# Optimization experiments

Hardware: AMD Instinct MI355X
Metric: run time of the kernel (lower is better)

The kernel has to match this reference:

```python
import jax, jax.numpy as jnp
import numpy as np

NEG_INF = float(np.finfo(np.float32).min)
EPS = 1e-6
NOISE_STD = 1.0
CHUNK = 8
TEMP = 1.0


def moving_sum(x, back, forward):
    # x: [B, T]; windowed sum over [t-back, t+forward] via prefix sums (O(T))
    B, T = x.shape
    cs = jnp.concatenate([jnp.zeros((B, 1), x.dtype), jnp.cumsum(x, axis=1)], axis=1)  # [B, T+1]
    idx = jnp.arange(T)
    hi = jnp.clip(idx + forward + 1, 0, T)
    lo = jnp.clip(idx - back, 0, T)
    return cs[:, hi] - cs[:, lo]


def setup_inputs() -> dict:
    key = jax.random.key(0)
    ks = jax.random.split(key, 12)
    B, T, KD, QD, AD, VD = 16, 4000, 512, 512, 512, 512
    s = lambda d: 1.0 / np.sqrt(d)
    return {
        "key": jax.random.normal(ks[0], (B, T, KD), jnp.float32),
        "value": jax.random.normal(ks[1], (B, T, VD), jnp.float32),
        "query": jax.random.normal(ks[2], (B, 1, QD), jnp.float32),
        "mask": jnp.ones((B, 1, T), jnp.int32),
        "w_key_mono": jax.random.normal(ks[3], (KD, AD), jnp.float32) * s(KD),
        "b_key_mono": jnp.zeros((AD,), jnp.float32),
        "w_query_mono": jax.random.normal(ks[4], (QD, AD), jnp.float32) * s(QD),
        "v_mono": jax.random.normal(ks[5], (AD,), jnp.float32) * s(AD),
        "g_mono": jnp.asarray(np.sqrt(1.0 / AD), jnp.float32),  # weight_norm gain init
        "r_mono": jnp.asarray(-4.0, jnp.float32),
        "w_key_chunk": jax.random.normal(ks[6], (KD, AD), jnp.float32) * s(KD),
        "b_key_chunk": jnp.zeros((AD,), jnp.float32),
        "w_query_chunk": jax.random.normal(ks[7], (QD, AD), jnp.float32) * s(QD),
        "v_chunk": jax.random.normal(ks[8], (AD,), jnp.float32) * s(AD),
    }


def _energy(key, query, mask, wk, bk, wq, v, r=None, g=None):
    kproj = jax.nn.relu(key) @ wk + bk          # [B, T, A]
    qproj = query @ wq                           # [B, 1, A]
    if g is not None:  # weight-normalized v
        v = g * v / jnp.linalg.norm(v)
    e = jnp.tanh(kproj + qproj) @ v              # [B, T]
    if r is not None:
        e = e + r
    return jnp.where(mask[:, 0, :] == 0, NEG_INF, e)


def reference(key, value, query, mask, w_key_mono, b_key_mono, w_query_mono, v_mono,
              g_mono, r_mono, w_key_chunk, b_key_chunk, w_query_chunk, v_chunk):
    B, T, _ = key.shape
    e_mono = _energy(key, query, mask, w_key_mono, b_key_mono, w_query_mono,
                     v_mono, r=r_mono, g=g_mono)
    noise = jax.random.normal(jax.random.key(123), e_mono.shape, e_mono.dtype) * NOISE_STD
    p_choose = jax.nn.sigmoid(e_mono + noise)                      # [B, T]
    # safe_cumprod of (1 - p): exp(exclusive cumsum of clipped logs)
    log1mp = jnp.log(jnp.clip(1.0 - p_choose, EPS, 1.0))
    cumprod_1mp = jnp.exp(jnp.cumsum(log1mp, axis=1) - log1mp)     # exclusive
    aw_prev = jnp.zeros((B, T), key.dtype).at[:, 0].set(1.0)       # one-hot at t=0
    alpha = p_choose * cumprod_1mp * jnp.cumsum(
        aw_prev / jnp.clip(cumprod_1mp, EPS, 1.0), axis=1)
    # chunkwise attention
    e_chunk = _energy(key, query, mask, w_key_chunk, b_key_chunk, w_query_chunk, v_chunk)
    e_chunk = e_chunk - jnp.max(e_chunk, axis=1, keepdims=True)
    softmax_exp = jnp.maximum(jnp.exp(e_chunk), 1e-5)
    denom = moving_sum(softmax_exp, CHUNK - 1, 0)
    beta = softmax_exp * moving_sum(alpha * TEMP / denom, 0, CHUNK - 1)
    cv = jnp.einsum('bt,btd->bd', beta, value)[:, None, :]         # [B, 1, V]
    return cv, alpha[..., None]
```

## Files before the change

### kernel.cpp

```cpp
#include <hip/hip_runtime.h>
#include <stdint.h>

typedef unsigned short u16;
typedef unsigned int   u32;

#define T_LEN 4000
#define NEG_INF (-3.4028234663852886e38f)

typedef __bf16 bf16x8 __attribute__((ext_vector_type(8)));
typedef float  f32x4  __attribute__((ext_vector_type(4)));

__device__ __forceinline__ u16 f2bf(float f){
    union { float f; u32 i; } v; v.f = f;
    u32 u = v.i;
    u32 r = (u + 0x7FFFu + ((u >> 16) & 1u)) >> 16;
    return (u16)r;
}
__device__ __forceinline__ float tanh_fast(float x){
    float ax = fabsf(x);
    float a = __expf(-2.0f * ax);
    float t = (1.0f - a) / (1.0f + a);
    return copysignf(t, x);
}
__device__ __forceinline__ u32 rotl32(u32 x, int n){ return (x << n) | (x >> (32 - n)); }

__device__ float jax_noise(u32 idx){
    const u32 k0 = 0u, k1 = 123u;
    const u32 k2 = k0 ^ k1 ^ 0x1BD11BDAu;
    u32 x0 = k0;
    u32 x1 = idx + k1;
#define RND(r) { x0 += x1; x1 = rotl32(x1, r); x1 ^= x0; }
    RND(13) RND(15) RND(26) RND(6)   x0 += k1; x1 += k2 + 1u;
    RND(17) RND(29) RND(16) RND(24)  x0 += k2; x1 += k0 + 2u;
    RND(13) RND(15) RND(26) RND(6)   x0 += k0; x1 += k1 + 3u;
    RND(17) RND(29) RND(16) RND(24)  x0 += k1; x1 += k2 + 4u;
    RND(13) RND(15) RND(26) RND(6)   x0 += k2; x1 += k0 + 5u;
#undef RND
    u32 bits = x0 ^ x1;
    union { u32 i; float f; } u;
    u.i = (bits >> 9) | 0x3F800000u;
    float f01 = u.f - 1.0f;
    const float minval = -0.99999994f;
    float uu = f01 * (1.0f - minval) + minval;
    uu = fmaxf(uu, minval);
    return 1.41421356f * erfinvf(uu);
}

__global__ __launch_bounds__(512) void prep_all(
    const float* __restrict__ v_mono, const float* __restrict__ g_mono,
    const float* __restrict__ query, const float* __restrict__ wq_mono,
    const float* __restrict__ wq_chunk,
    const float* __restrict__ wk_mono, const float* __restrict__ wk_chunk,
    float* __restrict__ vn, float* __restrict__ qp_mono, float* __restrict__ qp_chunk,
    u16* __restrict__ Wt)
{
    __shared__ float shf[512];
    __shared__ u16 tile[32][33];
    const int blk = blockIdx.x;
    const int tid = threadIdx.x;
    if (blk == 0){
        float v = v_mono[tid];
        shf[tid] = v * v;
        __syncthreads();
        for (int off = 256; off >= 1; off >>= 1){
            if (tid < off) shf[tid] += shf[tid + off];
            __syncthreads();
        }
        float g = g_mono[0];
        vn[tid] = g * v / sqrtf(shf[0]);
    } else if (blk <= 32){
        int b = (blk - 1) >> 1;
        int which = (blk - 1) & 1;
        const float* W = which ? wq_chunk : wq_mono;
        float* out = which ? qp_chunk : qp_mono;
        shf[tid] = query[b * 512 + tid];
        __syncthreads();
        float acc = 0.f;
        for (int k = 0; k < 512; k++) acc += shf[k] * W[k * 512 + tid];
        out[b * 512 + tid] = acc;
    } else {
        int idx = blk - 33;
        int kt = (idx & 15) * 32, nt = (idx >> 4) * 32;
        int c = tid & 31, r = tid >> 5;
        const float* src = (nt < 512) ? wk_mono : wk_chunk;
        int nbase = (nt < 512) ? nt : nt - 512;
#pragma unroll
        for (int i = 0; i < 2; i++){
            int kk = r + i * 16;
            tile[kk][c] = f2bf(src[(size_t)(kt + kk) * 512 + nbase + c]);
        }
        __syncthreads();
#pragma unroll
        for (int i = 0; i < 2; i++){
            int nn = r + i * 16;
            Wt[(size_t)(nt + nn) * 512 + kt + c] = tile[c][nn];
        }
    }
}

__global__ __launch_bounds__(256) void prep_key(const float* __restrict__ key,
                                                u16* __restrict__ kb){
    size_t i = ((size_t)blockIdx.x * 256 + threadIdx.x) * 8;
    float4 a = *reinterpret_cast<const float4*>(key + i);
    float4 b = *reinterpret_cast<const float4*>(key + i + 4);
    uint4 pk;
    pk.x = (u32)f2bf(fmaxf(a.x, 0.f)) | ((u32)f2bf(fmaxf(a.y, 0.f)) << 16);
    pk.y = (u32)f2bf(fmaxf(a.z, 0.f)) | ((u32)f2bf(fmaxf(a.w, 0.f)) << 16);
    pk.z = (u32)f2bf(fmaxf(b.x, 0.f)) | ((u32)f2bf(fmaxf(b.y, 0.f)) << 16);
    pk.w = (u32)f2bf(fmaxf(b.z, 0.f)) | ((u32)f2bf(fmaxf(b.w, 0.f)) << 16);
    *reinterpret_cast<uint4*>(kb + i) = pk;
}

template<bool PRE>
__global__ __launch_bounds__(256) void gemm_energy(
    const float* __restrict__ key, const u16* __restrict__ kb,
    const u16* __restrict__ Wt,
    const float* __restrict__ b_mono, const float* __restrict__ b_chunk,
    const float* __restrict__ vnorm, const float* __restrict__ v_chunk,
    const float* __restrict__ qp_mono, const float* __restrict__ qp_chunk,
    float* __restrict__ e_mono, float* __restrict__ e_chunk)
{
    __shared__ __align__(16) u16 As[128 * 40];
    __shared__ __align__(16) u16 Bs[128 * 40];
    const int tid = threadIdx.x;
    const int g0 = blockIdx.x * 128;
    const int nT = blockIdx.y;
    const bool mono = (nT < 4);
    const int n0 = nT * 128;
    const int lane = tid & 63;
    const int wave = tid >> 6;
    const int wm = wave >> 1, wn = wave & 1;
    const int l15 = lane & 15, quad = lane >> 4;

    f32x4 acc[4][4];
#pragma unroll
    for (int i = 0; i < 4; i++)
#pragma unroll
        for (int j = 0; j < 4; j++)
#pragma unroll
            for (int c = 0; c < 4; c++) acc[i][j][c] = 0.f;

    for (int k0 = 0; k0 < 512; k0 += 32){
        __syncthreads();
        if (PRE){
#pragma unroll
            for (int it = 0; it < 2; it++){
                int vid = tid + it * 256;
                int row = vid >> 2;
                int cb  = (vid & 3) << 3;
                uint4 a = *reinterpret_cast<const uint4*>(kb + (size_t)(g0 + row) * 512 + k0 + cb);
                *reinterpret_cast<uint4*>(&As[row * 40 + cb]) = a;
            }
        } else {
#pragma unroll
            for (int it = 0; it < 4; it++){
                int vid = tid + it * 256;
                int row = vid >> 3;
                int c4  = (vid & 7) << 2;
                float4 a = *reinterpret_cast<const float4*>(key + (size_t)(g0 + row) * 512 + k0 + c4);
                u32 p0 = (u32)f2bf(fmaxf(a.x, 0.f)) | ((u32)f2bf(fmaxf(a.y, 0.f)) << 16);
                u32 p1 = (u32)f2bf(fmaxf(a.z, 0.f)) | ((u32)f2bf(fmaxf(a.w, 0.f)) << 16);
                uint2 pk; pk.x = p0; pk.y = p1;
                *reinterpret_cast<uint2*>(&As[row * 40 + c4]) = pk;
            }
        }
#pragma unroll
        for (int it = 0; it < 2; it++){
            int vid = tid + it * 256;
            int row = vid >> 2;
            int cb  = (vid & 3) << 3;
            uint4 b = *reinterpret_cast<const uint4*>(Wt + (size_t)(n0 + row) * 512 + k0 + cb);
            *reinterpret_cast<uint4*>(&Bs[row * 40 + cb]) = b;
        }
        __syncthreads();
        bf16x8 af[4], bfr[4];
#pragma unroll
        for (int i = 0; i < 4; i++){
            af[i]  = *reinterpret_cast<const bf16x8*>(&As[(wm * 64 + i * 16 + l15) * 40 + quad * 8]);
            bfr[i] = *reinterpret_cast<const bf16x8*>(&Bs[(wn * 64 + i * 16 + l15) * 40 + quad * 8]);
        }
#pragma unroll
        for (int i = 0; i < 4; i++)
#pragma unroll
            for (int j = 0; j < 4; j++)
                acc[i][j] = __builtin_amdgcn_mfma_f32_16x16x32_bf16(af[i], bfr[j], acc[i][j], 0, 0, 0);
    }

    const float* qp = mono ? qp_mono : qp_chunk;
    float* edst = mono ? e_mono : e_chunk;
    float vv[4], bb[4]; int nc[4];
#pragma unroll
    for (int j = 0; j < 4; j++){
        int ncol = (n0 - (mono ? 0 : 512)) + wn * 64 + j * 16 + l15;
        nc[j] = ncol;
        vv[j] = mono ? vnorm[ncol] : v_chunk[ncol];
        bb[j] = mono ? b_mono[ncol] : b_chunk[ncol];
    }
#pragma unroll
    for (int i = 0; i < 4; i++){
#pragma unroll
        for (int r = 0; r < 4; r++){
            int g = g0 + wm * 64 + i * 16 + quad * 4 + r;
            int bidx = (u32)g / 4000u;
            float s = 0.f;
#pragma unroll
            for (int j = 0; j < 4; j++){
                float x = acc[i][j][r] + bb[j] + qp[bidx * 512 + nc[j]];
                s += vv[j] * tanh_fast(x);
            }
            s += __shfl_xor(s, 1);
            s += __shfl_xor(s, 2);
            s += __shfl_xor(s, 4);
            s += __shfl_xor(s, 8);
            if (l15 == 0) atomicAdd(&edst[g], s);
        }
    }
}

__global__ __launch_bounds__(256) void scan_energy(
    const float* __restrict__ e_mono, const float* __restrict__ e_chunk,
    const int* __restrict__ mask, const float* __restrict__ r_mono,
    float* __restrict__ out_alpha, float* __restrict__ beta)
{
    __shared__ float P[T_LEN];
    __shared__ float AL[T_LEN];
    __shared__ float SE[T_LEN];
    __shared__ float red[256];
    const int b = blockIdx.x;
    const int tid = threadIdx.x;
    const float r = r_mono[0];
    const int t0 = tid * 16;

    float l[16];
    float lsum = 0.f;
#pragma unroll
    for (int i = 0; i < 16; i++){
        int t = t0 + i;
        if (t < T_LEN){
            int fl = b * T_LEN + t;
            float e = e_mono[fl] + r;
            if (mask[fl] == 0) e = NEG_INF;
            float x = e + jax_noise((u32)fl);
            float p = 1.0f / (1.0f + expf(-x));
            P[t] = p;
            float om = 1.0f - p;
            om = fminf(fmaxf(om, 1e-6f), 1.0f);
            l[i] = logf(om);
            lsum += l[i];
        } else l[i] = 0.f;
    }
    red[tid] = lsum;
    __syncthreads();
#pragma unroll
    for (int off = 1; off < 256; off <<= 1){
        float v = (tid >= off) ? red[tid - off] : 0.f;
        __syncthreads();
        red[tid] += v;
        __syncthreads();
    }
    float run = red[tid] - lsum;
#pragma unroll
    for (int i = 0; i < 16; i++){
        int t = t0 + i;
        if (t < T_LEN){
            float alpha = P[t] * expf(run);
            run += l[i];
            AL[t] = alpha;
            out_alpha[b * T_LEN + t] = alpha;
        }
    }

    float ec[16]; float lmax = NEG_INF;
#pragma unroll
    for (int i = 0; i < 16; i++){
        int t = t0 + i;
        if (t < T_LEN){
            int fl = b * T_LEN + t;
            float e = e_chunk[fl];
            if (mask[fl] == 0) e = NEG_INF;
            ec[i] = e;
            lmax = fmaxf(lmax, e);
        } else ec[i] = NEG_INF;
    }
    __syncthreads();
    red[tid] = lmax;
    __syncthreads();
    for (int off = 128; off >= 1; off >>= 1){
        if (tid < off) red[tid] = fmaxf(red[tid], red[tid + off]);
        __syncthreads();
    }
    float m = red[0];
#pragma unroll
    for (int i = 0; i < 16; i++){
        int t = t0 + i;
        if (t < T_LEN) SE[t] = fmaxf(expf(ec[i] - m), 1e-5f);
    }
    __syncthreads();
#pragma unroll
    for (int i = 0; i < 16; i++){
        int t = t0 + i;
        if (t < T_LEN){
            float d = 0.f;
            int lo = t - 7; if (lo < 0) lo = 0;
            for (int s = lo; s <= t; s++) d += SE[s];
            P[t] = AL[t] / d;
        }
    }
    __syncthreads();
#pragma unroll
    for (int i = 0; i < 16; i++){
        int t = t0 + i;
        if (t < T_LEN){
            float s2 = 0.f;
            int hi = t + 7; if (hi > T_LEN - 1) hi = T_LEN - 1;
            for (int s = t; s <= hi; s++) s2 += P[s];
            beta[b * T_LEN + t] = SE[t] * s2;
        }
    }
}

__global__ __launch_bounds__(256) void cv_accum(const float* __restrict__ value,
                                                const float* __restrict__ beta,
                                                float* __restrict__ outcv){
    const int b = blockIdx.x >> 4;
    const int c = blockIdx.x & 15;
    const int tid = threadIdx.x;
    __shared__ float bsh[250];
    int tstart = c * 250;
    if (tid < 250) bsh[tid] = beta[b * T_LEN + tstart + tid];
    __syncthreads();
    int dl = (tid & 127) * 4;
    int trow = tid >> 7;
    float4 a = {0.f, 0.f, 0.f, 0.f};
    for (int t = trow; t < 250; t += 2){
        float bt = bsh[t];
        float4 v = *reinterpret_cast<const float4*>(
            value + (size_t)(b * T_LEN + tstart + t) * 512 + dl);
        a.x += bt * v.x; a.y += bt * v.y; a.z += bt * v.z; a.w += bt * v.w;
    }
    atomicAdd(&outcv[b * 512 + dl + 0], a.x);
    atomicAdd(&outcv[b * 512 + dl + 1], a.y);
    atomicAdd(&outcv[b * 512 + dl + 2], a.z);
    atomicAdd(&outcv[b * 512 + dl + 3], a.w);
}

extern "C" void kernel_launch(void* const* d_in, const int* in_sizes, int n_in,
                              void* d_out, int out_size, void* d_ws, size_t ws_size,
                              hipStream_t stream)
{
    const float* key      = (const float*)d_in[0];
    const float* value    = (const float*)d_in[1];
    const float* query    = (const float*)d_in[2];
    const int*   mask     = (const int*)d_in[3];
    const float* wk_mono  = (const float*)d_in[4];
    const float* bk_mono  = (const float*)d_in[5];
    const float* wq_mono  = (const float*)d_in[6];
    const float* v_mono   = (const float*)d_in[7];
    const float* g_mono   = (const float*)d_in[8];
    const float* r_mono   = (const float*)d_in[9];
    const float* wk_chunk = (const float*)d_in[10];
    const float* bk_chunk = (const float*)d_in[11];
    const float* wq_chunk = (const float*)d_in[12];
    const float* v_chunk  = (const float*)d_in[13];

    float* ws      = (float*)d_ws;
    float* e_mono  = ws;
    float* e_chunk = ws + 64000;
    float* beta    = ws + 136192;
    float* qp_mono = ws + 200192;
    float* qp_chunk= ws + 208384;
    float* vnorm   = ws + 216576;
    u16*   Wt      = (u16*)(ws + 217088);
    u16*   kb      = (u16*)(ws + 479232);

    const size_t NEED = 479232u * 4u + (size_t)64000 * 512 * 2;
    const bool big = ws_size >= NEED;

    hipMemsetAsync(ws, 0, 128000 * sizeof(float), stream);
    hipMemsetAsync(d_out, 0, 8192 * sizeof(float), stream);

    prep_all<<<545, 512, 0, stream>>>(v_mono, g_mono, query, wq_mono, wq_chunk,
                                      wk_mono, wk_chunk, vnorm, qp_mono, qp_chunk, Wt);
    if (big){
        prep_key<<<16000, 256, 0, stream>>>(key, kb);
        gemm_energy<true><<<dim3(500, 8), 256, 0, stream>>>(key, kb, Wt, bk_mono, bk_chunk,
                                                            vnorm, v_chunk, qp_mono, qp_chunk,
                                                            e_mono, e_chunk);
    } else {
        gemm_energy<false><<<dim3(500, 8), 256, 0, stream>>>(key, kb, Wt, bk_mono, bk_chunk,
                                                             vnorm, v_chunk, qp_mono, qp_chunk,
                                                             e_mono, e_chunk);
    }
    scan_energy<<<16, 256, 0, stream>>>(e_mono, e_chunk, mask, r_mono,
                                        (float*)d_out + 8192, beta);
    cv_accum<<<256, 256, 0, stream>>>(value, beta, (float*)d_out);
}
```

Before: 516.4 us.

## Fuse prep kernels and memsets, use direct-to-LDS loads and swizzled GEMM grid

Merges the weight prep, key bf16 conversion and the two memsets into one launch, which removes several kernel and memset launches. The pre-converted GEMM path now loads A and B tiles with global_load_lds straight into unpadded LDS, and remaps block ids so groups of 8 row tiles share each of the 8 column tiles for better L2 reuse. The scan kernel pads its shared arrays to avoid bank conflicts. Risks: unpadded LDS tiles may cause bank conflicts on the fragment reads, and the single-buffered loop still waits on each load before computing.

```diff
diff --git a/kernel.cpp b/kernel.cpp
--- a/kernel.cpp
+++ b/kernel.cpp
@@ -23,6 +23,12 @@
     return copysignf(t, x);
 }
 __device__ __forceinline__ u32 rotl32(u32 x, int n){ return (x << n) | (x >> (32 - n)); }
+
+__device__ __forceinline__ void gll16(const void* g, void* l){
+    __builtin_amdgcn_global_load_lds(
+        (__attribute__((address_space(1))) void*)g,
+        (__attribute__((address_space(3))) void*)l, 16, 0, 0);
+}
 
 __device__ float jax_noise(u32 idx){
     const u32 k0 = 0u, k1 = 123u;
@@ -46,13 +52,15 @@
     return 1.41421356f * erfinvf(uu);
 }
 
-__global__ __launch_bounds__(512) void prep_all(
+__global__ __launch_bounds__(512) void prep_combined(
     const float* __restrict__ v_mono, const float* __restrict__ g_mono,
     const float* __restrict__ query, const float* __restrict__ wq_mono,
     const float* __restrict__ wq_chunk,
     const float* __restrict__ wk_mono, const float* __restrict__ wk_chunk,
+    const float* __restrict__ key,
     float* __restrict__ vn, float* __restrict__ qp_mono, float* __restrict__ qp_chunk,
-    u16* __restrict__ Wt)
+    u16* __restrict__ Wt, u16* __restrict__ kb,
+    float* __restrict__ ezero, float* __restrict__ outcv)
 {
     __shared__ float shf[512];
     __shared__ u16 tile[32][33];
@@ -78,7 +86,7 @@
         float acc = 0.f;
         for (int k = 0; k < 512; k++) acc += shf[k] * W[k * 512 + tid];
         out[b * 512 + tid] = acc;
-    } else {
+    } else if (blk <= 544){
         int idx = blk - 33;
         int kt = (idx & 15) * 32, nt = (idx >> 4) * 32;
         int c = tid & 31, r = tid >> 5;
@@ -95,26 +103,119 @@
             int nn = r + i * 16;
             Wt[(size_t)(nt + nn) * 512 + kt + c] = tile[c][nn];
         }
-    }
-}
-
-__global__ __launch_bounds__(256) void prep_key(const float* __restrict__ key,
-                                                u16* __restrict__ kb){
-    size_t i = ((size_t)blockIdx.x * 256 + threadIdx.x) * 8;
-    float4 a = *reinterpret_cast<const float4*>(key + i);
-    float4 b = *reinterpret_cast<const float4*>(key + i + 4);
-    uint4 pk;
-    pk.x = (u32)f2bf(fmaxf(a.x, 0.f)) | ((u32)f2bf(fmaxf(a.y, 0.f)) << 16);
-    pk.y = (u32)f2bf(fmaxf(a.z, 0.f)) | ((u32)f2bf(fmaxf(a.w, 0.f)) << 16);
-    pk.z = (u32)f2bf(fmaxf(b.x, 0.f)) | ((u32)f2bf(fmaxf(b.y, 0.f)) << 16);
-    pk.w = (u32)f2bf(fmaxf(b.z, 0.f)) | ((u32)f2bf(fmaxf(b.w, 0.f)) << 16);
-    *reinterpret_cast<uint4*>(kb + i) = pk;
-}
-
-template<bool PRE>
-__global__ __launch_bounds__(256) void gemm_energy(
-    const float* __restrict__ key, const u16* __restrict__ kb,
-    const u16* __restrict__ Wt,
+    } else if (blk < 608){
+        int i = ((blk - 545) * 512 + tid) * 4;
+        if (i < 128000){
+            float4 z = {0.f, 0.f, 0.f, 0.f};
+            *reinterpret_cast<float4*>(ezero + i) = z;
+        }
+    } else if (blk < 612){
+        int i = ((blk - 608) * 512 + tid) * 4;
+        float4 z = {0.f, 0.f, 0.f, 0.f};
+        *reinterpret_cast<float4*>(outcv + i) = z;
+    } else {
+        size_t i = ((size_t)(blk - 612) * 512 + tid) * 8;
+        float4 a = *reinterpret_cast<const float4*>(key + i);
+        float4 b = *reinterpret_cast<const float4*>(key + i + 4);
+        uint4 pk;
+        pk.x = (u32)f2bf(fmaxf(a.x, 0.f)) | ((u32)f2bf(fmaxf(a.y, 0.f)) << 16);
+        pk.y = (u32)f2bf(fmaxf(a.z, 0.f)) | ((u32)f2bf(fmaxf(a.w, 0.f)) << 16);
+        pk.z = (u32)f2bf(fmaxf(b.x, 0.f)) | ((u32)f2bf(fmaxf(b.y, 0.f)) << 16);
+        pk.w = (u32)f2bf(fmaxf(b.z, 0.f)) | ((u32)f2bf(fmaxf(b.w, 0.f)) << 16);
+        *reinterpret_cast<uint4*>(kb + i) = pk;
+    }
+}
+
+__global__ __launch_bounds__(256) void gemm_energy_pre(
+    const u16* __restrict__ kb, const u16* __restrict__ Wt,
+    const float* __restrict__ b_mono, const float* __restrict__ b_chunk,
+    const float* __restrict__ vnorm, const float* __restrict__ v_chunk,
+    const float* __restrict__ qp_mono, const float* __restrict__ qp_chunk,
+    float* __restrict__ e_mono, float* __restrict__ e_chunk)
+{
+    __shared__ __align__(16) u16 As[128 * 32];
+    __shared__ __align__(16) u16 Bs[128 * 32];
+    const int bid = blockIdx.x;
+    const int x = ((bid >> 6) << 3) + (bid & 7);
+    if (x >= 500) return;
+    const int nT = (bid >> 3) & 7;
+    const int g0 = x * 128;
+    const bool mono = (nT < 4);
+    const int n0 = nT * 128;
+    const int tid = threadIdx.x;
+    const int lane = tid & 63;
+    const int wave = tid >> 6;
+    const int wm = wave >> 1, wn = wave & 1;
+    const int l15 = lane & 15, quad = lane >> 4;
+
+    f32x4 acc[4][4];
+#pragma unroll
+    for (int i = 0; i < 4; i++)
+#pragma unroll
+        for (int j = 0; j < 4; j++)
+#pragma unroll
+            for (int c = 0; c < 4; c++) acc[i][j][c] = 0.f;
+
+    const u16* aG = kb + (size_t)g0 * 512;
+    const u16* bG = Wt + (size_t)n0 * 512;
+
+    for (int k0 = 0; k0 < 512; k0 += 32){
+#pragma unroll
+        for (int it = 0; it < 2; it++){
+            int vid = tid + it * 256;
+            int row = vid >> 2;
+            int part = vid & 3;
+            gll16(aG + (size_t)row * 512 + k0 + part * 8, As + vid * 8);
+            gll16(bG + (size_t)row * 512 + k0 + part * 8, Bs + vid * 8);
+        }
+        __syncthreads();
+        bf16x8 af[4], bfr[4];
+#pragma unroll
+        for (int i = 0; i < 4; i++){
+            af[i]  = *reinterpret_cast<const bf16x8*>(&As[(wm * 64 + i * 16 + l15) * 32 + quad * 8]);
+            bfr[i] = *reinterpret_cast<const bf16x8*>(&Bs[(wn * 64 + i * 16 + l15) * 32 + quad * 8]);
+        }
+#pragma unroll
+        for (int i = 0; i < 4; i++)
+#pragma unroll
+            for (int j = 0; j < 4; j++)
+                acc[i][j] = __builtin_amdgcn_mfma_f32_16x16x32_bf16(af[i], bfr[j], acc[i][j], 0, 0, 0);
+        __syncthreads();
+    }
+
+    const float* qp = mono ? qp_mono : qp_chunk;
+    float* edst = mono ? e_mono : e_chunk;
+    float vv[4], bb[4]; int nc[4];
+#pragma unroll
+    for (int j = 0; j < 4; j++){
+        int ncol = (n0 - (mono ? 0 : 512)) + wn * 64 + j * 16 + l15;
+        nc[j] = ncol;
+        vv[j] = mono ? vnorm[ncol] : v_chunk[ncol];
+        bb[j] = mono ? b_mono[ncol] : b_chunk[ncol];
+    }
+#pragma unroll
+    for (int i = 0; i < 4; i++){
+#pragma unroll
+        for (int r = 0; r < 4; r++){
+            int g = g0 + wm * 64 + i * 16 + quad * 4 + r;
+            int bidx = (u32)g / 4000u;
+            float s = 0.f;
+#pragma unroll
+            for (int j = 0; j < 4; j++){
+                float x2 = acc[i][j][r] + bb[j] + qp[bidx * 512 + nc[j]];
+                s += vv[j] * tanh_fast(x2);
+            }
+            s += __shfl_xor(s, 1);
+            s += __shfl_xor(s, 2);
+            s += __shfl_xor(s, 4);
+            s += __shfl_xor(s, 8);
+            if (l15 == 0) atomicAdd(&edst[g], s);
+        }
+    }
+}
+
+__global__ __launch_bounds__(256) void gemm_energy_f32(
+    const float* __restrict__ key, const u16* __restrict__ Wt,
     const float* __restrict__ b_mono, const float* __restrict__ b_chunk,
     const float* __restrict__ vnorm, const float* __restrict__ v_chunk,
     const float* __restrict__ qp_mono, const float* __restrict__ qp_chunk,
@@ -142,27 +243,16 @@
 
     for (int k0 = 0; k0 < 512; k0 += 32){
         __syncthreads();
-        if (PRE){
-#pragma unroll
-            for (int it = 0; it < 2; it++){
-                int vid = tid + it * 256;
-                int row = vid >> 2;
-                int cb  = (vid & 3) << 3;
-                uint4 a = *reinterpret_cast<const uint4*>(kb + (size_t)(g0 + row) * 512 + k0 + cb);
-                *reinterpret_cast<uint4*>(&As[row * 40 + cb]) = a;
-            }
-        } else {
-#pragma unroll
-            for (int it = 0; it < 4; it++){
-                int vid = tid + it * 256;
-                int row = vid >> 3;
-                int c4  = (vid & 7) << 2;
-                float4 a = *reinterpret_cast<const float4*>(key + (size_t)(g0 + row) * 512 + k0 + c4);
-                u32 p0 = (u32)f2bf(fmaxf(a.x, 0.f)) | ((u32)f2bf(fmaxf(a.y, 0.f)) << 16);
-                u32 p1 = (u32)f2bf(fmaxf(a.z, 0.f)) | ((u32)f2bf(fmaxf(a.w, 0.f)) << 16);
-                uint2 pk; pk.x = p0; pk.y = p1;
-                *reinterpret_cast<uint2*>(&As[row * 40 + c4]) = pk;
-            }
+#pragma unroll
+        for (int it = 0; it < 4; it++){
+            int vid = tid + it * 256;
+            int row = vid >> 3;
+            int c4  = (vid & 7) << 2;
+            float4 a = *reinterpret_cast<const float4*>(key + (size_t)(g0 + row) * 512 + k0 + c4);
+            u32 p0 = (u32)f2bf(fmaxf(a.x, 0.f)) | ((u32)f2bf(fmaxf(a.y, 0.f)) << 16);
+            u32 p1 = (u32)f2bf(fmaxf(a.z, 0.f)) | ((u32)f2bf(fmaxf(a.w, 0.f)) << 16);
+            uint2 pk; pk.x = p0; pk.y = p1;
+            *reinterpret_cast<uint2*>(&As[row * 40 + c4]) = pk;
         }
 #pragma unroll
         for (int it = 0; it < 2; it++){
@@ -217,14 +307,16 @@
     }
 }
 
+#define IDX(t) ((t) + ((t) >> 4))
+
 __global__ __launch_bounds__(256) void scan_energy(
     const float* __restrict__ e_mono, const float* __restrict__ e_chunk,
     const int* __restrict__ mask, const float* __restrict__ r_mono,
     float* __restrict__ out_alpha, float* __restrict__ beta)
 {
-    __shared__ float P[T_LEN];
-    __shared__ float AL[T_LEN];
-    __shared__ float SE[T_LEN];
+    __shared__ float P[4256];
+    __shared__ float AL[4256];
+    __shared__ float SE[4256];
     __shared__ float red[256];
     const int b = blockIdx.x;
     const int tid = threadIdx.x;
@@ -242,7 +334,7 @@
             if (mask[fl] == 0) e = NEG_INF;
             float x = e + jax_noise((u32)fl);
             float p = 1.0f / (1.0f + expf(-x));
-            P[t] = p;
+            P[IDX(t)] = p;
             float om = 1.0f - p;
             om = fminf(fmaxf(om, 1e-6f), 1.0f);
             l[i] = logf(om);
@@ -263,9 +355,9 @@
     for (int i = 0; i < 16; i++){
         int t = t0 + i;
         if (t < T_LEN){
-            float alpha = P[t] * expf(run);
+            float alpha = P[IDX(t)] * expf(run);
             run += l[i];
-            AL[t] = alpha;
+            AL[IDX(t)] = alpha;
             out_alpha[b * T_LEN + t] = alpha;
         }
     }
@@ -293,7 +385,7 @@
 #pragma unroll
     for (int i = 0; i < 16; i++){
         int t = t0 + i;
-        if (t < T_LEN) SE[t] = fmaxf(expf(ec[i] - m), 1e-5f);
+        if (t < T_LEN) SE[IDX(t)] = fmaxf(expf(ec[i] - m), 1e-5f);
     }
     __syncthreads();
 #pragma unroll
@@ -302,8 +394,8 @@
         if (t < T_LEN){
             float d = 0.f;
             int lo = t - 7; if (lo < 0) lo = 0;
-            for (int s = lo; s <= t; s++) d += SE[s];
-            P[t] = AL[t] / d;
+            for (int s = lo; s <= t; s++) d += SE[IDX(s)];
+            P[IDX(t)] = AL[IDX(t)] / d;
         }
     }
     __syncthreads();
@@ -313,8 +405,8 @@
         if (t < T_LEN){
             float s2 = 0.f;
             int hi = t + 7; if (hi > T_LEN - 1) hi = T_LEN - 1;
-            for (int s = t; s <= hi; s++) s2 += P[s];
-            beta[b * T_LEN + t] = SE[t] * s2;
+            for (int s = t; s <= hi; s++) s2 += P[IDX(s)];
+            beta[b * T_LEN + t] = SE[IDX(t)] * s2;
         }
     }
 }
@@ -376,20 +468,18 @@
     const size_t NEED = 479232u * 4u + (size_t)64000 * 512 * 2;
     const bool big = ws_size >= NEED;
 
-    hipMemsetAsync(ws, 0, 128000 * sizeof(float), stream);
-    hipMemsetAsync(d_out, 0, 8192 * sizeof(float), stream);
-
-    prep_all<<<545, 512, 0, stream>>>(v_mono, g_mono, query, wq_mono, wq_chunk,
-                                      wk_mono, wk_chunk, vnorm, qp_mono, qp_chunk, Wt);
+    prep_combined<<<big ? 8612 : 612, 512, 0, stream>>>(
+        v_mono, g_mono, query, wq_mono, wq_chunk, wk_mono, wk_chunk, key,
+        vnorm, qp_mono, qp_chunk, Wt, kb, e_mono, (float*)d_out);
+
     if (big){
-        prep_key<<<16000, 256, 0, stream>>>(key, kb);
-        gemm_energy<true><<<dim3(500, 8), 256, 0, stream>>>(key, kb, Wt, bk_mono, bk_chunk,
-                                                            vnorm, v_chunk, qp_mono, qp_chunk,
-                                                            e_mono, e_chunk);
+        gemm_energy_pre<<<4096, 256, 0, stream>>>(kb, Wt, bk_mono, bk_chunk,
+                                                  vnorm, v_chunk, qp_mono, qp_chunk,
+                                                  e_mono, e_chunk);
     } else {
-        gemm_energy<false><<<dim3(500, 8), 256, 0, stream>>>(key, kb, Wt, bk_mono, bk_chunk,
-                                                             vnorm, v_chunk, qp_mono, qp_chunk,
-                                                             e_mono, e_chunk);
+        gemm_energy_f32<<<dim3(500, 8), 256, 0, stream>>>(key, Wt, bk_mono, bk_chunk,
+                                                          vnorm, v_chunk, qp_mono, qp_chunk,
+                                                          e_mono, e_chunk);
     }
     scan_energy<<<16, 256, 0, stream>>>(e_mono, e_chunk, mask, r_mono,
                                         (float*)d_out + 8192, beta);
```

After: 476.6 us. 1.08x faster.
